# Kernel tuning notes

Measured on AMD Instinct MI355X. Metric: run time of the kernel, lower is better.

Reference implementation:

```python
import jax, jax.numpy as jnp
import numpy as np
from jax import lax

T, D, I, E = 4096, 1024, 1024, 32
TOP_K = 4
ROUTED_SCALING = 1.0
EPS = 1e-6


def setup_inputs() -> dict:
    key = jax.random.key(0)
    k1, k2, k3, k4, k5 = jax.random.split(key, 5)
    return {
        "hidden_states": jax.random.normal(k1, (T, D), dtype=jnp.float32),
        "gate_w": jax.random.normal(k2, (E, D), dtype=jnp.float32) * 0.02,
        "gate_up_proj": jax.random.normal(k3, (E, 2 * I, D), dtype=jnp.float32) * 0.02,
        "down_proj": jax.random.normal(k4, (E, D, I), dtype=jnp.float32) * 0.02,
        "expert_bias": jax.random.normal(k5, (E,), dtype=jnp.float32) * 0.01,
    }


def _route(hidden_states, gate_w, expert_bias):
    # router_logits: [T, E]
    logits = hidden_states @ gate_w.T
    routing_weights = jax.nn.sigmoid(logits)
    # expert bias affects selection only, not the weights
    scores = routing_weights + expert_bias[None, :]
    _, selected = lax.top_k(scores, TOP_K)                      # [T, K] int32
    w = jnp.take_along_axis(routing_weights, selected, axis=1)  # [T, K]
    w = w / (w.sum(axis=-1, keepdims=True) + EPS)               # norm_topk_prob
    w = w * ROUTED_SCALING
    return selected, w


def reference(hidden_states, gate_w, gate_up_proj, down_proj, expert_bias):
    t, d = hidden_states.shape
    selected, w = _route(hidden_states, gate_w, expert_bias)
    # dense token->expert combine weights [T, E] (top_k indices are unique per row)
    comb = jnp.zeros((t, E), dtype=hidden_states.dtype)
    comb = comb.at[jnp.arange(t)[:, None], selected].add(w)

    def body(acc, xs):
        w_gu, w_d, cw = xs                       # [2I,D], [D,I], [T]
        gu = hidden_states @ w_gu.T              # [T, 2I]
        g, u = jnp.split(gu, 2, axis=-1)
        h = jax.nn.silu(g) * u                   # [T, I]
        out = h @ w_d.T                          # [T, D]
        return acc + out * cw[:, None], None

    init = jnp.zeros_like(hidden_states)
    final, _ = lax.scan(body, init, (gate_up_proj, down_proj, comb.T))
    return final
```

## Files before the change

kernel.cpp:

```cpp
#include <hip/hip_runtime.h>
#include <hip/hip_bf16.h>
#include <cstdint>
#include <cstddef>

#define T_TOK 4096
#define DIM   1024
#define IDIM  1024
#define NEXP  32
#define TOPK  4
#define MAXT  160
#define RPAD  (MAXT*128)

#define GUP_ELEMS 67108864ull
#define ALL_ELEMS 100663296ull
#define CONV_BLOCKS 49152
#define ROUTER_BLOCKS (T_TOK/4)

typedef short sh8  __attribute__((ext_vector_type(8)));
typedef float f32x4 __attribute__((ext_vector_type(4)));

__device__ __forceinline__ short bf(float f) {
    union { float f; uint32_t u; } v; v.f = f;
    uint32_t r = (v.u + 0x7FFFu + ((v.u >> 16) & 1u)) >> 16;
    return (short)r;
}
__device__ __forceinline__ float bf2f(short s) {
    union { uint32_t u; float f; } v; v.u = ((uint32_t)(uint16_t)s) << 16;
    return v.f;
}
__device__ __forceinline__ sh8 pack8(float4 a, float4 b) {
    sh8 r;
    r[0]=bf(a.x); r[1]=bf(a.y); r[2]=bf(a.z); r[3]=bf(a.w);
    r[4]=bf(b.x); r[5]=bf(b.y); r[6]=bf(b.z); r[7]=bf(b.w);
    return r;
}
__device__ __forceinline__ void glds16(const void* g, const void* l) {
    __builtin_amdgcn_global_load_lds((const __attribute__((address_space(1))) void*)g,
                                     (__attribute__((address_space(3))) void*)l, 16, 0, 0);
}

__device__ __forceinline__ int tile_expert(const int* __restrict__ cnt, int mt, int& tile_start) {
    int s = 0, e = -1, ts = 0;
    #pragma unroll
    for (int i = 0; i < NEXP; ++i) {
        int t = (cnt[i] + 127) >> 7;
        if (mt >= s && mt < s + t) { e = i; ts = s; }
        s += t;
    }
    tile_start = ts;
    return e;
}

template<bool DO_CONV>
__global__ __launch_bounds__(256) void front_kernel(
    const float* __restrict__ X, const float* __restrict__ GW,
    const float* __restrict__ bias,
    const float* __restrict__ gup, const float* __restrict__ dp,
    short* __restrict__ wgu, short* __restrict__ wd,
    int* __restrict__ topk_idx, float* __restrict__ topk_w,
    int* __restrict__ cnt, int* __restrict__ tlist_c, int* __restrict__ posmap)
{
    if (DO_CONV && blockIdx.x < CONV_BLOCKS) {
        size_t i = ((size_t)blockIdx.x * 256 + threadIdx.x) * 8;
        const float* src; short* dst;
        if (i < GUP_ELEMS) { src = gup + i; dst = wgu + i; }
        else               { src = dp + (i - GUP_ELEMS); dst = wd + (i - GUP_ELEMS); }
        float4 a = *reinterpret_cast<const float4*>(src);
        float4 b = *reinterpret_cast<const float4*>(src + 4);
        *reinterpret_cast<sh8*>(dst) = pack8(a, b);
        return;
    }
    int rb = DO_CONV ? (int)blockIdx.x - CONV_BLOCKS : (int)blockIdx.x;

    int wid  = threadIdx.x >> 6;
    int lane = threadIdx.x & 63;
    int t = rb * 4 + wid;

    float4 h[4];
    const float4* xr = reinterpret_cast<const float4*>(X + (size_t)t * DIM);
    #pragma unroll
    for (int c = 0; c < 4; ++c) h[c] = xr[lane + 64 * c];

    float myscore = 0.f;
    for (int e = 0; e < NEXP; ++e) {
        const float4* gr = reinterpret_cast<const float4*>(GW + (size_t)e * DIM);
        float p = 0.f;
        #pragma unroll
        for (int c = 0; c < 4; ++c) {
            float4 g = gr[lane + 64 * c];
            p += h[c].x * g.x + h[c].y * g.y + h[c].z * g.z + h[c].w * g.w;
        }
        #pragma unroll
        for (int o = 32; o; o >>= 1) p += __shfl_xor(p, o);
        if (lane == e) myscore = p;
    }
    float rw = 1.f / (1.f + expf(-myscore));
    float sel = (lane < NEXP) ? rw + bias[lane] : -1e30f;

    float wsum = 0.f;
    int   oi = 0; float ow = 0.f;
    #pragma unroll
    for (int k = 0; k < TOPK; ++k) {
        float v = sel;
        int   idx = (lane < NEXP) ? lane : 9999;
        #pragma unroll
        for (int o = 32; o; o >>= 1) {
            float v2 = __shfl_xor(v, o);
            int   i2 = __shfl_xor(idx, o);
            if (v2 > v || (v2 == v && i2 < idx)) { v = v2; idx = i2; }
        }
        float wk = __shfl(rw, idx);
        wsum += wk;
        if (lane == k)   { oi = idx; ow = wk; }
        if (lane == idx) sel = -1e30f;
    }
    if (lane < TOPK) {
        int gid = t * TOPK + lane;
        topk_idx[gid] = oi;
        topk_w  [gid] = ow / (wsum + 1e-6f);
        int pos = atomicAdd(&cnt[oi], 1);
        tlist_c[oi * T_TOK + pos] = t;
        posmap[gid] = pos;
    }
}

template<bool DO_XG>
__global__ __launch_bounds__(256) void gather_kernel(
    const float* __restrict__ X, const int* __restrict__ cnt,
    const int* __restrict__ tlist_c,
    short* __restrict__ Xg, int* __restrict__ tlist_p)
{
    int wid = threadIdx.x >> 6, lane = threadIdx.x & 63;
    int r = blockIdx.x * 4 + wid;
    int ts;
    int e = tile_expert(cnt, r >> 7, ts);
    if (e < 0) return;
    int li = r - (ts << 7);
    bool real = li < cnt[e];
    int t = real ? tlist_c[e * T_TOK + li] : 0;
    if (lane == 0) tlist_p[r] = t;
    if (DO_XG) {
        const float4* src = reinterpret_cast<const float4*>(X + (size_t)t * DIM);
        sh8* dst = reinterpret_cast<sh8*>(Xg + (size_t)r * DIM);
        float4 z = make_float4(0.f, 0.f, 0.f, 0.f);
        #pragma unroll
        for (int it = 0; it < 2; ++it) {
            int si = it * 64 + lane;
            float4 a = real ? src[2 * si]     : z;
            float4 b = real ? src[2 * si + 1] : z;
            dst[si] = pack8(a, b);
        }
    }
}

template<bool A_GLDS, bool W_BF16>
__global__ __launch_bounds__(256, 4) void gemm1_kernel(
    const short* __restrict__ Xg, const float* __restrict__ X,
    const short* __restrict__ Wgu, const float* __restrict__ GUP,
    const int* __restrict__ cnt, const int* __restrict__ tlist_p,
    short* __restrict__ H)
{
    int bid = (blockIdx.x & 7) * (MAXT * 16 / 8) + (blockIdx.x >> 3);
    int mt = bid >> 4;
    int nt = bid & 15;
    int ts;
    int e = tile_expert(cnt, mt, ts);
    if (e < 0) return;
    int m0 = mt * 128, n0 = nt * 64;

    __shared__ short As[128 * 64];
    __shared__ short Bg[64 * 64];
    __shared__ short Bu[64 * 64];

    int tid = threadIdx.x, lane = tid & 63, wv = tid >> 6;
    int wm = (wv >> 1) * 64, wn = (wv & 1) * 32;

    f32x4 accg[4][2] = {};
    f32x4 accu[4][2] = {};

    int swcol = ((lane & 7) ^ (lane >> 3)) * 8;
    const float* xrow = nullptr; int arow = 0, acol = 0;
    if (!A_GLDS) {
        arow = tid >> 1; acol = (tid & 1) * 32;
        xrow = X + (size_t)tlist_p[m0 + arow] * DIM;
    }
    const float *grow = nullptr, *urow = nullptr;
    int brow = tid >> 2, bcol = (tid & 3) * 16;
    if (!W_BF16) {
        grow = GUP + ((size_t)e * 2 * IDIM + n0 + brow) * DIM;
        urow = GUP + ((size_t)e * 2 * IDIM + IDIM + n0 + brow) * DIM;
    }
    const short* gb = Wgu + ((size_t)e * 2 * IDIM + n0) * DIM;
    const short* ub = Wgu + ((size_t)e * 2 * IDIM + IDIM + n0) * DIM;

    auto stage = [&](int k0) {
        if (A_GLDS) {
            #pragma unroll
            for (int j = 0; j < 4; ++j) {
                int ch = wv * 4 + j;
                glds16(Xg + (size_t)(m0 + ch * 8 + (lane >> 3)) * DIM + k0 + swcol, &As[ch * 512]);
            }
        } else {
            #pragma unroll
            for (int j = 0; j < 4; ++j) {
                int c = acol + j * 8;
                float4 a  = *reinterpret_cast<const float4*>(xrow + k0 + c);
                float4 bv = *reinterpret_cast<const float4*>(xrow + k0 + c + 4);
                *reinterpret_cast<sh8*>(&As[arow * 64 + (c ^ ((arow & 7) << 3))]) = pack8(a, bv);
            }
        }
        if (W_BF16) {
            #pragma unroll
            for (int j = 0; j < 2; ++j) {
                int ch = wv * 2 + j;
                glds16(gb + (size_t)(ch * 8 + (lane >> 3)) * DIM + k0 + swcol, &Bg[ch * 512]);
                glds16(ub + (size_t)(ch * 8 + (lane >> 3)) * DIM + k0 + swcol, &Bu[ch * 512]);
            }
        } else {
            #pragma unroll
            for (int j = 0; j < 2; ++j) {
                int c = bcol + j * 8;
                float4 a  = *reinterpret_cast<const float4*>(grow + k0 + c);
                float4 bv = *reinterpret_cast<const float4*>(grow + k0 + c + 4);
                *reinterpret_cast<sh8*>(&Bg[brow * 64 + (c ^ ((brow & 7) << 3))]) = pack8(a, bv);
                a  = *reinterpret_cast<const float4*>(urow + k0 + c);
                bv = *reinterpret_cast<const float4*>(urow + k0 + c + 4);
                *reinterpret_cast<sh8*>(&Bu[brow * 64 + (c ^ ((brow & 7) << 3))]) = pack8(a, bv);
            }
        }
    };

    int swr = (lane & 7) << 3;
    for (int it = 0; it < DIM / 64; ++it) {
        stage(it * 64);
        __syncthreads();
        #pragma unroll
        for (int kk = 0; kk < 64; kk += 32) {
            int ki = (kk + (lane >> 4) * 8) ^ swr;
            sh8 af[4], gf[2], uf[2];
            #pragma unroll
            for (int fm = 0; fm < 4; ++fm)
                af[fm] = *reinterpret_cast<const sh8*>(&As[(wm + fm * 16 + (lane & 15)) * 64 + ki]);
            #pragma unroll
            for (int fn = 0; fn < 2; ++fn) {
                gf[fn] = *reinterpret_cast<const sh8*>(&Bg[(wn + fn * 16 + (lane & 15)) * 64 + ki]);
                uf[fn] = *reinterpret_cast<const sh8*>(&Bu[(wn + fn * 16 + (lane & 15)) * 64 + ki]);
            }
            #pragma unroll
            for (int fm = 0; fm < 4; ++fm)
                #pragma unroll
                for (int fn = 0; fn < 2; ++fn) {
                    accg[fm][fn] = __builtin_amdgcn_mfma_f32_16x16x32_bf16(af[fm], gf[fn], accg[fm][fn], 0, 0, 0);
                    accu[fm][fn] = __builtin_amdgcn_mfma_f32_16x16x32_bf16(af[fm], uf[fn], accu[fm][fn], 0, 0, 0);
                }
        }
        __syncthreads();
    }

    #pragma unroll
    for (int fm = 0; fm < 4; ++fm)
        #pragma unroll
        for (int r = 0; r < 4; ++r) {
            int row = m0 + wm + fm * 16 + (lane >> 4) * 4 + r;
            #pragma unroll
            for (int fn = 0; fn < 2; ++fn) {
                int col = n0 + wn + fn * 16 + (lane & 15);
                float g = accg[fm][fn][r];
                float u = accu[fm][fn][r];
                H[(size_t)row * IDIM + col] = bf(g / (1.f + expf(-g)) * u);
            }
        }
}

template<bool W_BF16, bool Y_F32>
__global__ __launch_bounds__(256, 4) void gemm2_kernel(
    const short* __restrict__ H, const short* __restrict__ Wd, const float* __restrict__ DP,
    const int* __restrict__ cnt, float* __restrict__ Yf, short* __restrict__ Yb)
{
    int bid = (blockIdx.x & 7) * (MAXT * 8 / 8) + (blockIdx.x >> 3);
    int mt = bid >> 3;
    int nt = bid & 7;
    int ts;
    int e = tile_expert(cnt, mt, ts);
    if (e < 0) return;
    int m0 = mt * 128, n0 = nt * 128;

    __shared__ short As[128 * 64];
    __shared__ short Bs[128 * 64];

    int tid = threadIdx.x, lane = tid & 63, wv = tid >> 6;
    int wm = (wv >> 1) * 64, wn = (wv & 1) * 64;

    f32x4 acc[4][4] = {};

    int swcol = ((lane & 7) ^ (lane >> 3)) * 8;
    const float* drow = nullptr; int brow = 0, bcol = 0;
    if (!W_BF16) {
        brow = tid >> 1; bcol = (tid & 1) * 32;
        drow = DP + ((size_t)e * DIM + n0 + brow) * IDIM;
    }
    const short* db = Wd + ((size_t)e * DIM + n0) * IDIM;

    auto stage = [&](int k0) {
        #pragma unroll
        for (int j = 0; j < 4; ++j) {
            int ch = wv * 4 + j;
            glds16(H + (size_t)(m0 + ch * 8 + (lane >> 3)) * IDIM + k0 + swcol, &As[ch * 512]);
        }
        if (W_BF16) {
            #pragma unroll
            for (int j = 0; j < 4; ++j) {
                int ch = wv * 4 + j;
                glds16(db + (size_t)(ch * 8 + (lane >> 3)) * IDIM + k0 + swcol, &Bs[ch * 512]);
            }
        } else {
            #pragma unroll
            for (int j = 0; j < 4; ++j) {
                int c = bcol + j * 8;
                float4 a  = *reinterpret_cast<const float4*>(drow + k0 + c);
                float4 bv = *reinterpret_cast<const float4*>(drow + k0 + c + 4);
                *reinterpret_cast<sh8*>(&Bs[brow * 64 + (c ^ ((brow & 7) << 3))]) = pack8(a, bv);
            }
        }
    };

    int swr = (lane & 7) << 3;
    for (int it = 0; it < IDIM / 64; ++it) {
        stage(it * 64);
        __syncthreads();
        #pragma unroll
        for (int kk = 0; kk < 64; kk += 32) {
            int ki = (kk + (lane >> 4) * 8) ^ swr;
            sh8 af[4], bq[4];
            #pragma unroll
            for (int fm = 0; fm < 4; ++fm)
                af[fm] = *reinterpret_cast<const sh8*>(&As[(wm + fm * 16 + (lane & 15)) * 64 + ki]);
            #pragma unroll
            for (int fn = 0; fn < 4; ++fn)
                bq[fn] = *reinterpret_cast<const sh8*>(&Bs[(wn + fn * 16 + (lane & 15)) * 64 + ki]);
            #pragma unroll
            for (int fm = 0; fm < 4; ++fm)
                #pragma unroll
                for (int fn = 0; fn < 4; ++fn)
                    acc[fm][fn] = __builtin_amdgcn_mfma_f32_16x16x32_bf16(af[fm], bq[fn], acc[fm][fn], 0, 0, 0);
        }
        __syncthreads();
    }

    #pragma unroll
    for (int fm = 0; fm < 4; ++fm)
        #pragma unroll
        for (int r = 0; r < 4; ++r) {
            int row = m0 + wm + fm * 16 + (lane >> 4) * 4 + r;
            #pragma unroll
            for (int fn = 0; fn < 4; ++fn) {
                int col = n0 + wn + fn * 16 + (lane & 15);
                if (Y_F32) Yf[(size_t)row * DIM + col] = acc[fm][fn][r];
                else       Yb[(size_t)row * DIM + col] = bf(acc[fm][fn][r]);
            }
        }
}

template<bool Y_F32>
__global__ __launch_bounds__(256) void combine_kernel(
    const float* __restrict__ Yf, const short* __restrict__ Yb,
    const int* __restrict__ cnt, const int* __restrict__ topk_idx,
    const float* __restrict__ topk_w, const int* __restrict__ posmap,
    float* __restrict__ out)
{
    int t = blockIdx.x;
    int d = threadIdx.x * 4;
    int es[TOPK], rows[TOPK];
    #pragma unroll
    for (int k = 0; k < TOPK; ++k) es[k] = topk_idx[t * TOPK + k];
    int p = 0;
    #pragma unroll
    for (int i = 0; i < NEXP; ++i) {
        #pragma unroll
        for (int k = 0; k < TOPK; ++k)
            if (es[k] == i) rows[k] = p + posmap[t * TOPK + k];
        p += ((cnt[i] + 127) >> 7) << 7;
    }
    float4 acc = make_float4(0.f, 0.f, 0.f, 0.f);
    #pragma unroll
    for (int k = 0; k < TOPK; ++k) {
        float w = topk_w[t * TOPK + k];
        if (Y_F32) {
            float4 y = *reinterpret_cast<const float4*>(Yf + (size_t)rows[k] * DIM + d);
            acc.x += w * y.x; acc.y += w * y.y; acc.z += w * y.z; acc.w += w * y.w;
        } else {
            short4 y = *reinterpret_cast<const short4*>(Yb + (size_t)rows[k] * DIM + d);
            acc.x += w * bf2f(y.x); acc.y += w * bf2f(y.y);
            acc.z += w * bf2f(y.z); acc.w += w * bf2f(y.w);
        }
    }
    *reinterpret_cast<float4*>(out + (size_t)t * DIM + d) = acc;
}

extern "C" void kernel_launch(void* const* d_in, const int* in_sizes, int n_in,
                              void* d_out, int out_size, void* d_ws, size_t ws_size,
                              hipStream_t stream)
{
    const float* X    = (const float*)d_in[0];
    const float* GW   = (const float*)d_in[1];
    const float* GUP  = (const float*)d_in[2];
    const float* DP   = (const float*)d_in[3];
    const float* BIAS = (const float*)d_in[4];
    float* out = (float*)d_out;

    char* ws = (char*)d_ws;
    int*   cnt      = (int*)ws;
    int*   topk_idx = (int*)(ws + (4u   << 10));
    float* topk_w   = (float*)(ws + (68u  << 10));
    int*   posmap   = (int*)(ws + (132u << 10));
    int*   tlist_c  = (int*)(ws + (196u << 10));
    int*   tlist_p  = (int*)(ws + (708u << 10));

    constexpr size_t OFF_H   = 2ull << 20;
    constexpr size_t SZ_ROWS = (size_t)RPAD * IDIM * 2;
    constexpr size_t OFF_XG  = OFF_H + SZ_ROWS;
    constexpr size_t OFF_WGU = OFF_XG + SZ_ROWS;
    constexpr size_t OFF_WD  = OFF_WGU + GUP_ELEMS * 2;
    constexpr size_t END_ALL = OFF_WD + (ALL_ELEMS - GUP_ELEMS) * 2;
    constexpr size_t SZ_YF   = (size_t)RPAD * DIM * 4;

    short* H   = (short*)(ws + OFF_H);
    short* Xg  = (short*)(ws + OFF_XG);
    short* Wgu = (short*)(ws + OFF_WGU);
    short* Wd  = (short*)(ws + OFF_WD);
    float* Yf  = (float*)(ws + END_ALL);
    short* Yb  = Xg;

    bool t1   = ws_size >= END_ALL;
    bool t2   = ws_size >= OFF_WGU;
    bool yf32 = ws_size >= END_ALL + SZ_YF;

    (void)hipMemsetAsync(cnt, 0, 128, stream);

    if (t1) front_kernel<true ><<<CONV_BLOCKS + ROUTER_BLOCKS, 256, 0, stream>>>(
        X, GW, BIAS, GUP, DP, Wgu, Wd, topk_idx, topk_w, cnt, tlist_c, posmap);
    else    front_kernel<false><<<ROUTER_BLOCKS, 256, 0, stream>>>(
        X, GW, BIAS, GUP, DP, Wgu, Wd, topk_idx, topk_w, cnt, tlist_c, posmap);

    if (t2) gather_kernel<true ><<<RPAD / 4, 256, 0, stream>>>(X, cnt, tlist_c, Xg, tlist_p);
    else    gather_kernel<false><<<RPAD / 4, 256, 0, stream>>>(X, cnt, tlist_c, Xg, tlist_p);

    int g1 = MAXT * 16;
    if (t1)      gemm1_kernel<true , true ><<<g1, 256, 0, stream>>>(Xg, X, Wgu, GUP, cnt, tlist_p, H);
    else if (t2) gemm1_kernel<true , false><<<g1, 256, 0, stream>>>(Xg, X, Wgu, GUP, cnt, tlist_p, H);
    else         gemm1_kernel<false, false><<<g1, 256, 0, stream>>>(Xg, X, Wgu, GUP, cnt, tlist_p, H);

    int g2 = MAXT * 8;
    if (t1) {
        if (yf32) gemm2_kernel<true , true ><<<g2, 256, 0, stream>>>(H, Wd, DP, cnt, Yf, Yb);
        else      gemm2_kernel<true , false><<<g2, 256, 0, stream>>>(H, Wd, DP, cnt, Yf, Yb);
    } else {
        if (yf32) gemm2_kernel<false, true ><<<g2, 256, 0, stream>>>(H, Wd, DP, cnt, Yf, Yb);
        else      gemm2_kernel<false, false><<<g2, 256, 0, stream>>>(H, Wd, DP, cnt, Yf, Yb);
    }

    if (yf32) combine_kernel<true ><<<T_TOK, 256, 0, stream>>>(Yf, Yb, cnt, topk_idx, topk_w, posmap, out);
    else      combine_kernel<false><<<T_TOK, 256, 0, stream>>>(Yf, Yb, cnt, topk_idx, topk_w, posmap, out);
}
```

Before: 379.7 us.

## Drop per-call bf16 weight pre-conversion and convert fp32 weights inside GEMM staging

Removes the front pass that converted all expert weights (about 400MB of fp32) to bf16 on every call. The two GEMMs now read fp32 weights directly and pack them to bf16 in registers during staging. The tile schedule becomes weight-major, so each expert's N-tile blocks sit next to each other in launch order and share reused weight tiles through cache. Occupancy hints drop from 4 to 3. The trade is register-path weight staging instead of direct global-to-LDS loads, and the fp32 weights are read once per M-tile rather than once in total.

```diff
diff --git a/kernel.cpp b/kernel.cpp
--- a/kernel.cpp
+++ b/kernel.cpp
@@ -11,22 +11,13 @@
 #define MAXT  160
 #define RPAD  (MAXT*128)
 
-#define GUP_ELEMS 67108864ull
-#define ALL_ELEMS 100663296ull
-#define CONV_BLOCKS 49152
-#define ROUTER_BLOCKS (T_TOK/4)
-
-typedef short sh8  __attribute__((ext_vector_type(8)));
+typedef short sh8   __attribute__((ext_vector_type(8)));
 typedef float f32x4 __attribute__((ext_vector_type(4)));
 
 __device__ __forceinline__ short bf(float f) {
     union { float f; uint32_t u; } v; v.f = f;
     uint32_t r = (v.u + 0x7FFFu + ((v.u >> 16) & 1u)) >> 16;
     return (short)r;
-}
-__device__ __forceinline__ float bf2f(short s) {
-    union { uint32_t u; float f; } v; v.u = ((uint32_t)(uint16_t)s) << 16;
-    return v.f;
 }
 __device__ __forceinline__ sh8 pack8(float4 a, float4 b) {
     sh8 r;
@@ -51,30 +42,32 @@
     return e;
 }
 
-template<bool DO_CONV>
-__global__ __launch_bounds__(256) void front_kernel(
+__device__ __forceinline__ bool decode_wmajor(const int* __restrict__ cnt, int bid, int ntsz,
+                                              int& e, int& mt, int& nt) {
+    int base = 0, tacc = 0, fe = -1, floc = 0, fts = 0, fntl = 1;
+    #pragma unroll
+    for (int i = 0; i < NEXP; ++i) {
+        int ntl = (cnt[i] + 127) >> 7;
+        int sz  = ntsz * ntl;
+        if (bid >= base && bid < base + sz) { fe = i; floc = bid - base; fts = tacc; fntl = ntl; }
+        base += sz; tacc += ntl;
+    }
+    if (fe < 0) return false;
+    e  = fe;
+    nt = floc / fntl;
+    mt = fts + (floc % fntl);
+    return true;
+}
+
+__global__ __launch_bounds__(256) void router_kernel(
     const float* __restrict__ X, const float* __restrict__ GW,
-    const float* __restrict__ bias,
-    const float* __restrict__ gup, const float* __restrict__ dp,
-    short* __restrict__ wgu, short* __restrict__ wd,
-    int* __restrict__ topk_idx, float* __restrict__ topk_w,
-    int* __restrict__ cnt, int* __restrict__ tlist_c, int* __restrict__ posmap)
-{
-    if (DO_CONV && blockIdx.x < CONV_BLOCKS) {
-        size_t i = ((size_t)blockIdx.x * 256 + threadIdx.x) * 8;
-        const float* src; short* dst;
-        if (i < GUP_ELEMS) { src = gup + i; dst = wgu + i; }
-        else               { src = dp + (i - GUP_ELEMS); dst = wd + (i - GUP_ELEMS); }
-        float4 a = *reinterpret_cast<const float4*>(src);
-        float4 b = *reinterpret_cast<const float4*>(src + 4);
-        *reinterpret_cast<sh8*>(dst) = pack8(a, b);
-        return;
-    }
-    int rb = DO_CONV ? (int)blockIdx.x - CONV_BLOCKS : (int)blockIdx.x;
-
+    const float* __restrict__ bias, int* __restrict__ topk_idx,
+    float* __restrict__ topk_w, int* __restrict__ cnt,
+    int* __restrict__ tlist_c, int* __restrict__ posmap)
+{
     int wid  = threadIdx.x >> 6;
     int lane = threadIdx.x & 63;
-    int t = rb * 4 + wid;
+    int t = blockIdx.x * 4 + wid;
 
     float4 h[4];
     const float4* xr = reinterpret_cast<const float4*>(X + (size_t)t * DIM);
@@ -124,11 +117,9 @@
     }
 }
 
-template<bool DO_XG>
 __global__ __launch_bounds__(256) void gather_kernel(
     const float* __restrict__ X, const int* __restrict__ cnt,
-    const int* __restrict__ tlist_c,
-    short* __restrict__ Xg, int* __restrict__ tlist_p)
+    const int* __restrict__ tlist_c, short* __restrict__ Xg)
 {
     int wid = threadIdx.x >> 6, lane = threadIdx.x & 63;
     int r = blockIdx.x * 4 + wid;
@@ -138,34 +129,25 @@
     int li = r - (ts << 7);
     bool real = li < cnt[e];
     int t = real ? tlist_c[e * T_TOK + li] : 0;
-    if (lane == 0) tlist_p[r] = t;
-    if (DO_XG) {
-        const float4* src = reinterpret_cast<const float4*>(X + (size_t)t * DIM);
-        sh8* dst = reinterpret_cast<sh8*>(Xg + (size_t)r * DIM);
-        float4 z = make_float4(0.f, 0.f, 0.f, 0.f);
-        #pragma unroll
-        for (int it = 0; it < 2; ++it) {
-            int si = it * 64 + lane;
-            float4 a = real ? src[2 * si]     : z;
-            float4 b = real ? src[2 * si + 1] : z;
-            dst[si] = pack8(a, b);
-        }
-    }
-}
-
-template<bool A_GLDS, bool W_BF16>
-__global__ __launch_bounds__(256, 4) void gemm1_kernel(
-    const short* __restrict__ Xg, const float* __restrict__ X,
-    const short* __restrict__ Wgu, const float* __restrict__ GUP,
-    const int* __restrict__ cnt, const int* __restrict__ tlist_p,
-    short* __restrict__ H)
+    const float4* src = reinterpret_cast<const float4*>(X + (size_t)t * DIM);
+    sh8* dst = reinterpret_cast<sh8*>(Xg + (size_t)r * DIM);
+    float4 z = make_float4(0.f, 0.f, 0.f, 0.f);
+    #pragma unroll
+    for (int it = 0; it < 2; ++it) {
+        int si = it * 64 + lane;
+        float4 a = real ? src[2 * si]     : z;
+        float4 b = real ? src[2 * si + 1] : z;
+        dst[si] = pack8(a, b);
+    }
+}
+
+__global__ __launch_bounds__(256, 3) void gemm1_kernel(
+    const short* __restrict__ Xg, const float* __restrict__ GUP,
+    const int* __restrict__ cnt, short* __restrict__ H)
 {
     int bid = (blockIdx.x & 7) * (MAXT * 16 / 8) + (blockIdx.x >> 3);
-    int mt = bid >> 4;
-    int nt = bid & 15;
-    int ts;
-    int e = tile_expert(cnt, mt, ts);
-    if (e < 0) return;
+    int e, mt, nt;
+    if (!decode_wmajor(cnt, bid, 16, e, mt, nt)) return;
     int m0 = mt * 128, n0 = nt * 64;
 
     __shared__ short As[128 * 64];
@@ -179,54 +161,25 @@
     f32x4 accu[4][2] = {};
 
     int swcol = ((lane & 7) ^ (lane >> 3)) * 8;
-    const float* xrow = nullptr; int arow = 0, acol = 0;
-    if (!A_GLDS) {
-        arow = tid >> 1; acol = (tid & 1) * 32;
-        xrow = X + (size_t)tlist_p[m0 + arow] * DIM;
-    }
-    const float *grow = nullptr, *urow = nullptr;
     int brow = tid >> 2, bcol = (tid & 3) * 16;
-    if (!W_BF16) {
-        grow = GUP + ((size_t)e * 2 * IDIM + n0 + brow) * DIM;
-        urow = GUP + ((size_t)e * 2 * IDIM + IDIM + n0 + brow) * DIM;
-    }
-    const short* gb = Wgu + ((size_t)e * 2 * IDIM + n0) * DIM;
-    const short* ub = Wgu + ((size_t)e * 2 * IDIM + IDIM + n0) * DIM;
+    const float* grow = GUP + ((size_t)e * 2 * IDIM + n0 + brow) * DIM;
+    const float* urow = GUP + ((size_t)e * 2 * IDIM + IDIM + n0 + brow) * DIM;
 
     auto stage = [&](int k0) {
-        if (A_GLDS) {
-            #pragma unroll
-            for (int j = 0; j < 4; ++j) {
-                int ch = wv * 4 + j;
-                glds16(Xg + (size_t)(m0 + ch * 8 + (lane >> 3)) * DIM + k0 + swcol, &As[ch * 512]);
-            }
-        } else {
-            #pragma unroll
-            for (int j = 0; j < 4; ++j) {
-                int c = acol + j * 8;
-                float4 a  = *reinterpret_cast<const float4*>(xrow + k0 + c);
-                float4 bv = *reinterpret_cast<const float4*>(xrow + k0 + c + 4);
-                *reinterpret_cast<sh8*>(&As[arow * 64 + (c ^ ((arow & 7) << 3))]) = pack8(a, bv);
-            }
-        }
-        if (W_BF16) {
-            #pragma unroll
-            for (int j = 0; j < 2; ++j) {
-                int ch = wv * 2 + j;
-                glds16(gb + (size_t)(ch * 8 + (lane >> 3)) * DIM + k0 + swcol, &Bg[ch * 512]);
-                glds16(ub + (size_t)(ch * 8 + (lane >> 3)) * DIM + k0 + swcol, &Bu[ch * 512]);
-            }
-        } else {
-            #pragma unroll
-            for (int j = 0; j < 2; ++j) {
-                int c = bcol + j * 8;
-                float4 a  = *reinterpret_cast<const float4*>(grow + k0 + c);
-                float4 bv = *reinterpret_cast<const float4*>(grow + k0 + c + 4);
-                *reinterpret_cast<sh8*>(&Bg[brow * 64 + (c ^ ((brow & 7) << 3))]) = pack8(a, bv);
-                a  = *reinterpret_cast<const float4*>(urow + k0 + c);
-                bv = *reinterpret_cast<const float4*>(urow + k0 + c + 4);
-                *reinterpret_cast<sh8*>(&Bu[brow * 64 + (c ^ ((brow & 7) << 3))]) = pack8(a, bv);
-            }
+        #pragma unroll
+        for (int j = 0; j < 4; ++j) {
+            int ch = wv * 4 + j;
+            glds16(Xg + (size_t)(m0 + ch * 8 + (lane >> 3)) * DIM + k0 + swcol, &As[ch * 512]);
+        }
+        #pragma unroll
+        for (int j = 0; j < 2; ++j) {
+            int c = bcol + j * 8;
+            float4 a  = *reinterpret_cast<const float4*>(grow + k0 + c);
+            float4 bv = *reinterpret_cast<const float4*>(grow + k0 + c + 4);
+            *reinterpret_cast<sh8*>(&Bg[brow * 64 + (c ^ ((brow & 7) << 3))]) = pack8(a, bv);
+            a  = *reinterpret_cast<const float4*>(urow + k0 + c);
+            bv = *reinterpret_cast<const float4*>(urow + k0 + c + 4);
+            *reinterpret_cast<sh8*>(&Bu[brow * 64 + (c ^ ((brow & 7) << 3))]) = pack8(a, bv);
         }
     };
 
@@ -272,17 +225,13 @@
         }
 }
 
-template<bool W_BF16, bool Y_F32>
-__global__ __launch_bounds__(256, 4) void gemm2_kernel(
-    const short* __restrict__ H, const short* __restrict__ Wd, const float* __restrict__ DP,
-    const int* __restrict__ cnt, float* __restrict__ Yf, short* __restrict__ Yb)
+__global__ __launch_bounds__(256, 3) void gemm2_kernel(
+    const short* __restrict__ H, const float* __restrict__ DP,
+    const int* __restrict__ cnt, float* __restrict__ Yf)
 {
     int bid = (blockIdx.x & 7) * (MAXT * 8 / 8) + (blockIdx.x >> 3);
-    int mt = bid >> 3;
-    int nt = bid & 7;
-    int ts;
-    int e = tile_expert(cnt, mt, ts);
-    if (e < 0) return;
+    int e, mt, nt;
+    if (!decode_wmajor(cnt, bid, 8, e, mt, nt)) return;
     int m0 = mt * 128, n0 = nt * 128;
 
     __shared__ short As[128 * 64];
@@ -294,12 +243,8 @@
     f32x4 acc[4][4] = {};
 
     int swcol = ((lane & 7) ^ (lane >> 3)) * 8;
-    const float* drow = nullptr; int brow = 0, bcol = 0;
-    if (!W_BF16) {
-        brow = tid >> 1; bcol = (tid & 1) * 32;
-        drow = DP + ((size_t)e * DIM + n0 + brow) * IDIM;
-    }
-    const short* db = Wd + ((size_t)e * DIM + n0) * IDIM;
+    int brow = tid >> 1, bcol = (tid & 1) * 32;
+    const float* drow = DP + ((size_t)e * DIM + n0 + brow) * IDIM;
 
     auto stage = [&](int k0) {
         #pragma unroll
@@ -307,20 +252,12 @@
             int ch = wv * 4 + j;
             glds16(H + (size_t)(m0 + ch * 8 + (lane >> 3)) * IDIM + k0 + swcol, &As[ch * 512]);
         }
-        if (W_BF16) {
-            #pragma unroll
-            for (int j = 0; j < 4; ++j) {
-                int ch = wv * 4 + j;
-                glds16(db + (size_t)(ch * 8 + (lane >> 3)) * IDIM + k0 + swcol, &Bs[ch * 512]);
-            }
-        } else {
-            #pragma unroll
-            for (int j = 0; j < 4; ++j) {
-                int c = bcol + j * 8;
-                float4 a  = *reinterpret_cast<const float4*>(drow + k0 + c);
-                float4 bv = *reinterpret_cast<const float4*>(drow + k0 + c + 4);
-                *reinterpret_cast<sh8*>(&Bs[brow * 64 + (c ^ ((brow & 7) << 3))]) = pack8(a, bv);
-            }
+        #pragma unroll
+        for (int j = 0; j < 4; ++j) {
+            int c = bcol + j * 8;
+            float4 a  = *reinterpret_cast<const float4*>(drow + k0 + c);
+            float4 bv = *reinterpret_cast<const float4*>(drow + k0 + c + 4);
+            *reinterpret_cast<sh8*>(&Bs[brow * 64 + (c ^ ((brow & 7) << 3))]) = pack8(a, bv);
         }
     };
 
@@ -355,18 +292,15 @@
             #pragma unroll
             for (int fn = 0; fn < 4; ++fn) {
                 int col = n0 + wn + fn * 16 + (lane & 15);
-                if (Y_F32) Yf[(size_t)row * DIM + col] = acc[fm][fn][r];
-                else       Yb[(size_t)row * DIM + col] = bf(acc[fm][fn][r]);
+                Yf[(size_t)row * DIM + col] = acc[fm][fn][r];
             }
         }
 }
 
-template<bool Y_F32>
 __global__ __launch_bounds__(256) void combine_kernel(
-    const float* __restrict__ Yf, const short* __restrict__ Yb,
-    const int* __restrict__ cnt, const int* __restrict__ topk_idx,
-    const float* __restrict__ topk_w, const int* __restrict__ posmap,
-    float* __restrict__ out)
+    const float* __restrict__ Yf, const int* __restrict__ cnt,
+    const int* __restrict__ topk_idx, const float* __restrict__ topk_w,
+    const int* __restrict__ posmap, float* __restrict__ out)
 {
     int t = blockIdx.x;
     int d = threadIdx.x * 4;
@@ -385,14 +319,8 @@
     #pragma unroll
     for (int k = 0; k < TOPK; ++k) {
         float w = topk_w[t * TOPK + k];
-        if (Y_F32) {
-            float4 y = *reinterpret_cast<const float4*>(Yf + (size_t)rows[k] * DIM + d);
-            acc.x += w * y.x; acc.y += w * y.y; acc.z += w * y.z; acc.w += w * y.w;
-        } else {
-            short4 y = *reinterpret_cast<const short4*>(Yb + (size_t)rows[k] * DIM + d);
-            acc.x += w * bf2f(y.x); acc.y += w * bf2f(y.y);
-            acc.z += w * bf2f(y.z); acc.w += w * bf2f(y.w);
-        }
+        float4 y = *reinterpret_cast<const float4*>(Yf + (size_t)rows[k] * DIM + d);
+        acc.x += w * y.x; acc.y += w * y.y; acc.z += w * y.z; acc.w += w * y.w;
     }
     *reinterpret_cast<float4*>(out + (size_t)t * DIM + d) = acc;
 }
@@ -414,51 +342,24 @@
     float* topk_w   = (float*)(ws + (68u  << 10));
     int*   posmap   = (int*)(ws + (132u << 10));
     int*   tlist_c  = (int*)(ws + (196u << 10));
-    int*   tlist_p  = (int*)(ws + (708u << 10));
-
-    constexpr size_t OFF_H   = 2ull << 20;
-    constexpr size_t SZ_ROWS = (size_t)RPAD * IDIM * 2;
-    constexpr size_t OFF_XG  = OFF_H + SZ_ROWS;
-    constexpr size_t OFF_WGU = OFF_XG + SZ_ROWS;
-    constexpr size_t OFF_WD  = OFF_WGU + GUP_ELEMS * 2;
-    constexpr size_t END_ALL = OFF_WD + (ALL_ELEMS - GUP_ELEMS) * 2;
-    constexpr size_t SZ_YF   = (size_t)RPAD * DIM * 4;
-
-    short* H   = (short*)(ws + OFF_H);
-    short* Xg  = (short*)(ws + OFF_XG);
-    short* Wgu = (short*)(ws + OFF_WGU);
-    short* Wd  = (short*)(ws + OFF_WD);
-    float* Yf  = (float*)(ws + END_ALL);
-    short* Yb  = Xg;
-
-    bool t1   = ws_size >= END_ALL;
-    bool t2   = ws_size >= OFF_WGU;
-    bool yf32 = ws_size >= END_ALL + SZ_YF;
+
+    constexpr size_t OFF_H  = 2ull << 20;
+    constexpr size_t SZ_BF  = (size_t)RPAD * IDIM * 2;
+    constexpr size_t OFF_XG = OFF_H + SZ_BF;
+    constexpr size_t OFF_YF = OFF_XG + SZ_BF;
+
+    short* H  = (short*)(ws + OFF_H);
+    short* Xg = (short*)(ws + OFF_XG);
+    float* Yf = (float*)(ws + OFF_YF);
 
     (void)hipMemsetAsync(cnt, 0, 128, stream);
 
-    if (t1) front_kernel<true ><<<CONV_BLOCKS + ROUTER_BLOCKS, 256, 0, stream>>>(
-        X, GW, BIAS, GUP, DP, Wgu, Wd, topk_idx, topk_w, cnt, tlist_c, posmap);
-    else    front_kernel<false><<<ROUTER_BLOCKS, 256, 0, stream>>>(
-        X, GW, BIAS, GUP, DP, Wgu, Wd, topk_idx, topk_w, cnt, tlist_c, posmap);
-
-    if (t2) gather_kernel<true ><<<RPAD / 4, 256, 0, stream>>>(X, cnt, tlist_c, Xg, tlist_p);
-    else    gather_kernel<false><<<RPAD / 4, 256, 0, stream>>>(X, cnt, tlist_c, Xg, tlist_p);
-
-    int g1 = MAXT * 16;
-    if (t1)      gemm1_kernel<true , true ><<<g1, 256, 0, stream>>>(Xg, X, Wgu, GUP, cnt, tlist_p, H);
-    else if (t2) gemm1_kernel<true , false><<<g1, 256, 0, stream>>>(Xg, X, Wgu, GUP, cnt, tlist_p, H);
-    else         gemm1_kernel<false, false><<<g1, 256, 0, stream>>>(Xg, X, Wgu, GUP, cnt, tlist_p, H);
-
-    int g2 = MAXT * 8;
-    if (t1) {
-        if (yf32) gemm2_kernel<true , true ><<<g2, 256, 0, stream>>>(H, Wd, DP, cnt, Yf, Yb);
-        else      gemm2_kernel<true , false><<<g2, 256, 0, stream>>>(H, Wd, DP, cnt, Yf, Yb);
-    } else {
-        if (yf32) gemm2_kernel<false, true ><<<g2, 256, 0, stream>>>(H, Wd, DP, cnt, Yf, Yb);
-        else      gemm2_kernel<false, false><<<g2, 256, 0, stream>>>(H, Wd, DP, cnt, Yf, Yb);
-    }
-
-    if (yf32) combine_kernel<true ><<<T_TOK, 256, 0, stream>>>(Yf, Yb, cnt, topk_idx, topk_w, posmap, out);
-    else      combine_kernel<false><<<T_TOK, 256, 0, stream>>>(Yf, Yb, cnt, topk_idx, topk_w, posmap, out);
-}
+    router_kernel<<<T_TOK / 4, 256, 0, stream>>>(X, GW, BIAS, topk_idx, topk_w,
+                                                 cnt, tlist_c, posmap);
+    gather_kernel<<<RPAD / 4, 256, 0, stream>>>(X, cnt, tlist_c, Xg);
+
+    gemm1_kernel<<<MAXT * 16, 256, 0, stream>>>(Xg, GUP, cnt, H);
+    gemm2_kernel<<<MAXT * 8,  256, 0, stream>>>(H, DP, cnt, Yf);
+
+    combine_kernel<<<T_TOK, 256, 0, stream>>>(Yf, cnt, topk_idx, topk_w, posmap, out);
+}
```

Result: slower. 494.2 us (+30.1%).
